# Kernel optimization log

Hardware: AMD Instinct MI355X
Metric: run time of the kernel (lower is better)

The kernel has to match this reference:

```python
import jax, jax.numpy as jnp
import numpy as np

E, N, C, A, S, H, HD, RH = 320000, 20000, 128, 4, 16, 8, 32, 64
AH = H * HD  # 256 attn-head channels; mul_alpha = AH, mul_alpha_head = HD
OUT = 128


def smooth_leaky_relu(x, a=0.2):
    # Equiformer SmoothLeakyReLU: 0.5*((1+a)*x + (1-a)*x*(2*sigmoid(x)-1))
    return 0.5 * ((1 + a) * x + (1 - a) * x * (2.0 * jax.nn.sigmoid(x) - 1.0))


def setup_inputs() -> dict:
    key = jax.random.key(0)
    ks = jax.random.split(key, 20)
    d = {
        'message': jax.random.normal(ks[0], (E, C), jnp.float32),
        'edge_attr': jax.random.normal(ks[1], (E, A), jnp.float32),
        'edge_scalars': jax.random.normal(ks[2], (E, S), jnp.float32),
        'w_rad1': jax.random.normal(ks[3], (S, RH), jnp.float32) / np.sqrt(S),
        'b_rad1': jnp.zeros((RH,), jnp.float32),
        'w_rad2': jax.random.normal(ks[4], (RH, C * A), jnp.float32) / np.sqrt(RH),
        'b_rad2': jnp.zeros((C * A,), jnp.float32),
        'w_dtp_v': jax.random.normal(ks[5], (C, A), jnp.float32) / np.sqrt(A),
        'w_lin_act': jax.random.normal(ks[6], (C, C), jnp.float32) / np.sqrt(C),
        'b_lin_act': jnp.zeros((C,), jnp.float32),
        'w_alpha': jax.random.normal(ks[7], (C, AH), jnp.float32) / np.sqrt(C),
        'b_alpha': jnp.zeros((AH,), jnp.float32),
        'w_lin_v': jax.random.normal(ks[8], (C, AH), jnp.float32) / np.sqrt(C),
        'b_lin_v': jnp.zeros((AH,), jnp.float32),
        'alpha_dot': jax.random.normal(ks[9], (H, HD), jnp.float32) / np.sqrt(HD),
        'w_proj': jax.random.normal(ks[10], (AH, OUT), jnp.float32) / np.sqrt(AH),
        'b_proj': jnp.zeros((OUT,), jnp.float32),
        'edge_dst': jax.random.randint(ks[11], (E,), 0, N, jnp.int32),
        'n_nodes_dst': N,
    }
    return d


def reference(message, edge_attr, edge_scalars,
              w_rad1, b_rad1, w_rad2, b_rad2,
              w_dtp_v, w_lin_act, b_lin_act,
              w_alpha, b_alpha, w_lin_v, b_lin_v,
              alpha_dot, w_proj, b_proj,
              edge_dst, n_nodes_dst):
    n = n_nodes_dst
    # dtp_rad: radial MLP -> per-edge depthwise TP weights [E, C, A]
    h = jax.nn.silu(edge_scalars @ w_rad1 + b_rad1)
    w = (h @ w_rad2 + b_rad2).reshape(-1, C, A)
    # sep_act.dtp (scalar irreps): out[e,c] = msg[e,c] * sum_a w[e,c,a]*attr[e,a]
    msg = message * jnp.einsum('eca,ea->ec', w, edge_attr)
    # sep_alpha -> alpha heads [E, H, HD]
    alpha = (msg @ w_alpha + b_alpha).reshape(-1, H, HD)
    # sep_act.lin + gate (scalars -> SiLU)
    value = jax.nn.silu(msg @ w_lin_act + b_lin_act)
    # sep_value: internal-weight dtp then linear, reshape to heads
    value = value * jnp.einsum('ca,ea->ec', w_dtp_v, edge_attr)
    value = (value @ w_lin_v + b_lin_v).reshape(-1, H, HD)
    # attention logits
    alpha = smooth_leaky_relu(alpha)
    alpha = jnp.einsum('ehk,hk->eh', alpha, alpha_dot)
    # scatter softmax over destination nodes
    amax = jax.ops.segment_max(alpha, edge_dst, num_segments=n)  # [N, H]
    amax = jnp.where(jnp.isfinite(amax), amax, 0.0)
    ex = jnp.exp(alpha - amax[edge_dst])
    denom = jax.ops.segment_sum(ex, edge_dst, num_segments=n)
    alpha = ex / (denom[edge_dst] + 1e-16)
    # weighted scatter-add aggregation
    attn = value * alpha[..., None]  # [E, H, HD]
    node = jax.ops.segment_sum(attn, edge_dst, num_segments=n)  # [N, H, HD]
    node = node.reshape(n, AH)  # heads2vec
    return node @ w_proj + b_proj
```

## Files before the change

### kernel.cpp

```cpp
#include <hip/hip_runtime.h>

#define C_   128
#define A_   4
#define S_   16
#define RH_  64
#define H_   8
#define AH_  256
#define OUT_ 128

typedef __attribute__((ext_vector_type(8))) short bf16x8;
typedef __attribute__((ext_vector_type(4))) float f32x4;

__device__ __forceinline__ float sigf(float x) { return 1.0f / (1.0f + __expf(-x)); }

__device__ __forceinline__ unsigned short f2bf(float x) {
    unsigned u = __float_as_uint(x);
    unsigned r = (u + 0x7fffu + ((u >> 16) & 1u)) >> 16;
    return (unsigned short)r;
}

__device__ __forceinline__ unsigned enc(float x) {
    unsigned b = __float_as_uint(x);
    return (b & 0x80000000u) ? ~b : (b | 0x80000000u);
}
__device__ __forceinline__ float dec(unsigned u) {
    unsigned b = (u & 0x80000000u) ? (u & 0x7fffffffu) : ~u;
    return __uint_as_float(b);
}

__global__ void k_pack(const float* __restrict__ W, short* __restrict__ out, int K, int N) {
    const int KS = K / 32;
    const int ct = blockIdx.x / KS, ks = blockIdx.x % KS;
    const int l = threadIdx.x, lr = l & 15, lg = l >> 4;
    bf16x8 v;
    #pragma unroll
    for (int j = 0; j < 8; j++)
        v[j] = (short)f2bf(W[(size_t)(ks * 32 + lg * 8 + j) * N + ct * 16 + lr]);
    *(bf16x8*)&out[((size_t)blockIdx.x * 64 + l) * 8] = v;
}

__global__ void k_pack_dtp(const float* __restrict__ W, short* __restrict__ out) {
    const int ct = blockIdx.x >> 3, ks = blockIdx.x & 7;
    const int l = threadIdx.x, lr = l & 15, lg = l >> 4;
    bf16x8 v;
    #pragma unroll
    for (int j = 0; j < 8; j++)
        v[j] = (short)f2bf(W[(size_t)(ks * 8 + lg * 2 + (j >> 2)) * 512 + (ct * 16 + lr) * 4 + (j & 3)]);
    *(bf16x8*)&out[((size_t)blockIdx.x * 64 + l) * 8] = v;
}

__global__ __launch_bounds__(256) void k_hist(
    const int* __restrict__ edge_dst, int* __restrict__ deg, int E)
{
    const int e = blockIdx.x * 256 + threadIdx.x;
    if (e < E) atomicAdd(&deg[edge_dst[e]], 1);
}

__global__ __launch_bounds__(1024) void k_scan(
    const int* __restrict__ deg, int* __restrict__ base, int* __restrict__ cursor, int N)
{
    __shared__ int part[1024];
    const int t = threadIdx.x;
    const int per = (N + 1023) / 1024;
    const int i0 = t * per;
    int s = 0;
    for (int i = 0; i < per; i++) { int idx = i0 + i; if (idx < N) s += deg[idx]; }
    part[t] = s;
    __syncthreads();
    for (int off = 1; off < 1024; off <<= 1) {
        int v = (t >= off) ? part[t - off] : 0;
        __syncthreads();
        part[t] += v;
        __syncthreads();
    }
    int excl = (t == 0) ? 0 : part[t - 1];
    for (int i = 0; i < per; i++) {
        int idx = i0 + i;
        if (idx < N) { base[idx] = excl; cursor[idx] = excl; excl += deg[idx]; }
    }
}

__global__ __launch_bounds__(256) void k_fill(
    const int* __restrict__ edge_dst, int* __restrict__ cursor,
    int* __restrict__ sorted, int E)
{
    const int e = blockIdx.x * 256 + threadIdx.x;
    if (e < E) {
        const int pos = atomicAdd(&cursor[edge_dst[e]], 1);
        sorted[pos] = e;
    }
}

__global__ __launch_bounds__(512, 4) void k_msgalpha(
    const float* __restrict__ message, const float* __restrict__ edge_attr,
    const float* __restrict__ edge_scalars,
    const float* __restrict__ w_rad1, const float* __restrict__ b_rad1,
    const short* __restrict__ w_rad2_lin, const float* __restrict__ b_rad2,
    const short* __restrict__ w_alpha_lin, const float* __restrict__ b_alpha,
    const float* __restrict__ alpha_dot, const int* __restrict__ edge_dst,
    short* __restrict__ msg_bf, float* __restrict__ logits, unsigned* __restrict__ amax_u)
{
    __shared__ __align__(16) char smem[50432];
    short* Ap     = (short*)smem;
    short* msg_s  = (short*)(smem + 32768);
    float* w1_s   = (float*)(smem + 32768);
    float* es_s   = (float*)(smem + 32768 + 4096);
    float* attr_s = (float*)(smem + 49152);
    int*   dst_s  = (int*)(smem + 50176);

    const int t = threadIdx.x;
    const long e0 = (long)blockIdx.x * 64;

    if (t < 256) {
        *(float4*)&w1_s[t * 4] = *(const float4*)&w_rad1[t * 4];
    } else {
        const int i = t - 256, r = i >> 2, s4 = (i & 3) * 4;
        *(float4*)&es_s[r * 17 + s4] = *(const float4*)&edge_scalars[(e0 + r) * S_ + s4];
    }
    if (t < 64) {
        *(float4*)&attr_s[t * 4] = *(const float4*)&edge_attr[(e0 + t) * A_];
        dst_s[t] = edge_dst[e0 + t];
    }
    __syncthreads();

    {
        const int r = t & 63, o0 = (t >> 6) * 8;
        float acc[8];
        #pragma unroll
        for (int i = 0; i < 8; i++) acc[i] = b_rad1[o0 + i];
        #pragma unroll
        for (int s = 0; s < S_; s++) {
            const float ev = es_s[r * 17 + s];
            #pragma unroll
            for (int i = 0; i < 8; i++) acc[i] += ev * w1_s[s * 64 + o0 + i];
        }
        float h[8];
        #pragma unroll
        for (int i = 0; i < 8; i++) { const float x = acc[i]; h[i] = x * sigf(x); }
        const float4 a4 = *(const float4*)&attr_s[r * 4];
        char* base = (char*)Ap + r * 512;
        const int sw = (r & 31) << 4;
        #pragma unroll
        for (int c = 0; c < 4; c++) {
            const float h0 = h[2 * c], h1 = h[2 * c + 1];
            bf16x8 v;
            v[0] = (short)f2bf(h0 * a4.x); v[1] = (short)f2bf(h0 * a4.y);
            v[2] = (short)f2bf(h0 * a4.z); v[3] = (short)f2bf(h0 * a4.w);
            v[4] = (short)f2bf(h1 * a4.x); v[5] = (short)f2bf(h1 * a4.y);
            v[6] = (short)f2bf(h1 * a4.z); v[7] = (short)f2bf(h1 * a4.w);
            *(bf16x8*)(base + ((o0 * 8 + c * 16) ^ sw)) = v;
        }
    }
    __syncthreads();

    const int w = t >> 6, l = t & 63, lr = l & 15, lg = l >> 4;

    {
        bf16x8 bf[8];
        #pragma unroll
        for (int ks = 0; ks < 8; ks++)
            bf[ks] = *(const bf16x8*)&w_rad2_lin[((size_t)(w * 8 + ks) * 64 + l) * 8];
        const int col = w * 16 + lr;
        const float4 b2 = *(const float4*)&b_rad2[col * 4];
        #pragma unroll 1
        for (int rt = 0; rt < 4; rt++) {
            const int arow = rt * 16 + lr;
            const char* abase = (char*)Ap + arow * 512;
            const int asw = (arow & 31) << 4;
            bf16x8 af[8];
            #pragma unroll
            for (int ks = 0; ks < 8; ks++)
                af[ks] = *(const bf16x8*)(abase + ((ks * 64 + lg * 16) ^ asw));
            f32x4 acc = {0.f, 0.f, 0.f, 0.f};
            #pragma unroll
            for (int ks = 0; ks < 8; ks++)
                acc = __builtin_amdgcn_mfma_f32_16x16x32_bf16(af[ks], bf[ks], acc, 0, 0, 0);
            #pragma unroll
            for (int r = 0; r < 4; r++) {
                const int row = rt * 16 + lg * 4 + r;
                const float4 a4 = *(const float4*)&attr_s[row * 4];
                const float badj = a4.x * b2.x + a4.y * b2.y + a4.z * b2.z + a4.w * b2.w;
                const float m = message[(e0 + row) * C_ + col];
                *(short*)((char*)msg_s + row * 256 + ((col * 2) ^ ((row & 15) << 4))) =
                    (short)f2bf(m * (acc[r] + badj));
            }
        }
    }
    __syncthreads();

    {
        #pragma unroll
        for (int i = 0; i < 2; i++) {
            const int q = t + i * 512;
            const int row = q >> 4, ch = q & 15;
            const uint4 v = *(const uint4*)((char*)msg_s + row * 256 + ((ch * 16) ^ ((row & 15) << 4)));
            *(uint4*)((char*)msg_bf + ((e0 + row) * 256 + ch * 16)) = v;
        }
    }

    {
        bf16x8 waf[2][4];
        float4 ba4[2], ad4[2];
        #pragma unroll
        for (int q = 0; q < 2; q++) {
            const int rt = w * 2 + q;
            #pragma unroll
            for (int ks = 0; ks < 4; ks++)
                waf[q][ks] = *(const bf16x8*)&w_alpha_lin[((size_t)(rt * 4 + ks) * 64 + l) * 8];
            ba4[q] = *(const float4*)&b_alpha[rt * 16 + lg * 4];
            ad4[q] = *(const float4*)&alpha_dot[rt * 16 + lg * 4];
        }
        #pragma unroll 1
        for (int ct = 0; ct < 4; ct++) {
            const int erow = ct * 16 + lr;
            const char* mbase = (char*)msg_s + erow * 256;
            const int msw = (erow & 15) << 4;
            bf16x8 mb[4];
            #pragma unroll
            for (int ks = 0; ks < 4; ks++)
                mb[ks] = *(const bf16x8*)(mbase + ((ks * 64 + lg * 16) ^ msw));
            float s = 0.f;
            #pragma unroll
            for (int q = 0; q < 2; q++) {
                f32x4 acc = {0.f, 0.f, 0.f, 0.f};
                #pragma unroll
                for (int ks = 0; ks < 4; ks++)
                    acc = __builtin_amdgcn_mfma_f32_16x16x32_bf16(waf[q][ks], mb[ks], acc, 0, 0, 0);
                #pragma unroll
                for (int r = 0; r < 4; r++) {
                    const float x = acc[r] + ((const float*)&ba4[q])[r];
                    const float y = x * (0.2f + 0.8f * sigf(x));
                    s += y * ((const float*)&ad4[q])[r];
                }
            }
            s += __shfl_xor(s, 16);
            s += __shfl_xor(s, 32);
            if (lg == 0) {
                const long e = e0 + ct * 16 + lr;
                logits[e * H_ + w] = s;
                atomicMax(&amax_u[dst_s[ct * 16 + lr] * H_ + w], enc(s));
            }
        }
    }
}

__global__ __launch_bounds__(256) void k_denom(
    const float* __restrict__ logits, const int* __restrict__ edge_dst,
    const unsigned* __restrict__ amax_u, float* __restrict__ denom, int EH)
{
    const int t = blockIdx.x * 256 + threadIdx.x;
    if (t >= EH) return;
    const int e = t >> 3, h = t & 7;
    const int n = edge_dst[e];
    const float am = dec(amax_u[n * H_ + h]);
    atomicAdd(&denom[n * H_ + h], __expf(logits[t] - am));
}

__global__ __launch_bounds__(256) void k_value(
    const short* __restrict__ msg_bf, const float* __restrict__ edge_attr,
    const short* __restrict__ w_lin_act_lin, const float* __restrict__ b_lin_act,
    const float* __restrict__ w_dtp_v,
    const short* __restrict__ w_lin_v_lin, const float* __restrict__ b_lin_v,
    const float* __restrict__ logits, const int* __restrict__ edge_dst,
    const unsigned* __restrict__ amax_u, const float* __restrict__ denom,
    const int* __restrict__ sorted, float* __restrict__ node)
{
    __shared__ __align__(16) short a_s[32 * 128];
    __shared__ __align__(16) short v_s[32 * 128];
    __shared__ float val2[32 * 260];
    __shared__ float attr_s[32][4];
    __shared__ float wgt_s[32][H_];
    __shared__ int   dst_s[32];
    __shared__ int   eid_s[32];
    const int t = threadIdx.x;
    const int b0 = blockIdx.x * 32;

    if (t < 32) {
        const int e = sorted[b0 + t];
        eid_s[t] = e;
        dst_s[t] = edge_dst[e];
        *(float4*)&attr_s[t][0] = *(const float4*)&edge_attr[(long)e * A_];
    }
    __syncthreads();
    #pragma unroll
    for (int i = 0; i < 2; i++) {
        const int row = (t >> 4) + i * 16, ch = t & 15;
        const uint4 v = *(const uint4*)((const char*)msg_bf + ((long)eid_s[row] * 256 + ch * 16));
        *(uint4*)((char*)a_s + row * 256 + ((ch * 16) ^ ((row & 7) << 4))) = v;
    }
    {
        const int el = t >> 3, h = t & 7;
        const long e = eid_s[el];
        const int n = dst_s[el];
        const float am = dec(amax_u[n * H_ + h]);
        const float d  = denom[n * H_ + h];
        wgt_s[el][h] = __expf(logits[e * H_ + h] - am) / (d + 1e-16f);
    }
    __syncthreads();

    const int w = t >> 6, l = t & 63, lr = l & 15, lg = l >> 4;
    bf16x8 af[2][4];
    #pragma unroll
    for (int rt = 0; rt < 2; rt++)
        #pragma unroll
        for (int ks = 0; ks < 4; ks++) {
            const int row = rt * 16 + lr;
            af[rt][ks] = *(bf16x8*)((char*)a_s + row * 256 + ((ks * 64 + lg * 16) ^ ((row & 7) << 4)));
        }
    #pragma unroll
    for (int q = 0; q < 2; q++) {
        const int ct = w * 2 + q;
        bf16x8 bf[4];
        #pragma unroll
        for (int ks = 0; ks < 4; ks++)
            bf[ks] = *(const bf16x8*)&w_lin_act_lin[((size_t)(ct * 4 + ks) * 64 + l) * 8];
        const int col = ct * 16 + lr;
        const float bb = b_lin_act[col];
        const float4 wv = *(const float4*)&w_dtp_v[col * 4];
        #pragma unroll
        for (int rt = 0; rt < 2; rt++) {
            f32x4 acc = {0.f, 0.f, 0.f, 0.f};
            #pragma unroll
            for (int ks = 0; ks < 4; ks++)
                acc = __builtin_amdgcn_mfma_f32_16x16x32_bf16(af[rt][ks], bf[ks], acc, 0, 0, 0);
            #pragma unroll
            for (int r = 0; r < 4; r++) {
                const int row = rt * 16 + lg * 4 + r;
                float x = acc[r] + bb;
                x = x * sigf(x);
                const float4 a4 = *(const float4*)&attr_s[row][0];
                const float dv = wv.x * a4.x + wv.y * a4.y + wv.z * a4.z + wv.w * a4.w;
                *(short*)((char*)v_s + row * 256 + ((col * 2) ^ ((row & 7) << 4))) =
                    (short)f2bf(x * dv);
            }
        }
    }
    __syncthreads();

    bf16x8 vf[2][4];
    #pragma unroll
    for (int rt = 0; rt < 2; rt++)
        #pragma unroll
        for (int ks = 0; ks < 4; ks++) {
            const int row = rt * 16 + lr;
            vf[rt][ks] = *(bf16x8*)((char*)v_s + row * 256 + ((ks * 64 + lg * 16) ^ ((row & 7) << 4)));
        }
    #pragma unroll
    for (int q = 0; q < 4; q++) {
        const int ct = w * 4 + q;
        bf16x8 bf[4];
        #pragma unroll
        for (int ks = 0; ks < 4; ks++)
            bf[ks] = *(const bf16x8*)&w_lin_v_lin[((size_t)(ct * 4 + ks) * 64 + l) * 8];
        const int col = ct * 16 + lr;
        const float bb = b_lin_v[col];
        #pragma unroll
        for (int rt = 0; rt < 2; rt++) {
            f32x4 acc = {0.f, 0.f, 0.f, 0.f};
            #pragma unroll
            for (int ks = 0; ks < 4; ks++)
                acc = __builtin_amdgcn_mfma_f32_16x16x32_bf16(vf[rt][ks], bf[ks], acc, 0, 0, 0);
            #pragma unroll
            for (int r = 0; r < 4; r++) {
                const int row = rt * 16 + lg * 4 + r;
                val2[row * 260 + col] = (acc[r] + bb) * wgt_s[row][col >> 5];
            }
        }
    }
    __syncthreads();
    {
        const int c = t;
        float run = 0.f;
        int s = 0;
        #pragma unroll 1
        for (int e = 0; e < 32; e++) {
            run += val2[e * 260 + c];
            const bool end = (e == 31) || (dst_s[e + 1] != dst_s[e]);
            if (end) {
                float* np = node + (long)dst_s[e] * AH_ + c;
                if (s == 0 || e == 31) atomicAdd(np, run);
                else *np = run;
                run = 0.f; s = e + 1;
            }
        }
    }
}

__global__ __launch_bounds__(256) void k_proj(
    const float* __restrict__ node, const float* __restrict__ w_proj,
    const float* __restrict__ b_proj, float* __restrict__ out)
{
    __shared__ float node_s[32][AH_];
    const int t = threadIdx.x;
    const long n0 = (long)blockIdx.x * 32;
    #pragma unroll
    for (int i = 0; i < 8; i++) {
        const int idx = t + i * 256;
        const int nl = idx >> 6, c4 = (idx & 63) * 4;
        *(float4*)&node_s[nl][c4] = *(const float4*)&node[(n0 + nl) * AH_ + c4];
    }
    __syncthreads();
    const int j0 = (t & 31) * 4;
    const int g  = t >> 5;
    float4 acc4[4];
    const float4 b = *(const float4*)&b_proj[j0];
    #pragma unroll
    for (int i = 0; i < 4; i++) acc4[i] = b;
    const float* wp = w_proj + j0;
    for (int c4 = 0; c4 < 64; c4++) {
        const float4 w0 = *(const float4*)&wp[(c4 * 4 + 0) * OUT_];
        const float4 w1 = *(const float4*)&wp[(c4 * 4 + 1) * OUT_];
        const float4 w2 = *(const float4*)&wp[(c4 * 4 + 2) * OUT_];
        const float4 w3 = *(const float4*)&wp[(c4 * 4 + 3) * OUT_];
        #pragma unroll
        for (int i = 0; i < 4; i++) {
            const float4 nv = *(const float4*)&node_s[g * 4 + i][c4 * 4];
            acc4[i].x += nv.x * w0.x + nv.y * w1.x + nv.z * w2.x + nv.w * w3.x;
            acc4[i].y += nv.x * w0.y + nv.y * w1.y + nv.z * w2.y + nv.w * w3.y;
            acc4[i].z += nv.x * w0.z + nv.y * w1.z + nv.z * w2.z + nv.w * w3.z;
            acc4[i].w += nv.x * w0.w + nv.y * w1.w + nv.z * w2.w + nv.w * w3.w;
        }
    }
    #pragma unroll
    for (int i = 0; i < 4; i++) {
        const long n = n0 + g * 4 + i;
        *(float4*)&out[n * OUT_ + j0] = acc4[i];
    }
}

extern "C" void kernel_launch(void* const* d_in, const int* in_sizes, int n_in,
                              void* d_out, int out_size, void* d_ws, size_t ws_size,
                              hipStream_t stream)
{
    const float* message      = (const float*)d_in[0];
    const float* edge_attr    = (const float*)d_in[1];
    const float* edge_scalars = (const float*)d_in[2];
    const float* w_rad1       = (const float*)d_in[3];
    const float* b_rad1       = (const float*)d_in[4];
    const float* w_rad2       = (const float*)d_in[5];
    const float* b_rad2       = (const float*)d_in[6];
    const float* w_dtp_v      = (const float*)d_in[7];
    const float* w_lin_act    = (const float*)d_in[8];
    const float* b_lin_act    = (const float*)d_in[9];
    const float* w_alpha      = (const float*)d_in[10];
    const float* b_alpha      = (const float*)d_in[11];
    const float* w_lin_v      = (const float*)d_in[12];
    const float* b_lin_v      = (const float*)d_in[13];
    const float* alpha_dot    = (const float*)d_in[14];
    const float* w_proj       = (const float*)d_in[15];
    const float* b_proj       = (const float*)d_in[16];
    const int*   edge_dst     = (const int*)d_in[17];

    const int E = in_sizes[0] / C_;
    const int N = out_size / OUT_;

    char* ws = (char*)d_ws;
    float*    node     = (float*)ws;
    unsigned* amax_u   = (unsigned*)(node + (size_t)N * AH_);
    float*    denom    = (float*)(amax_u + (size_t)N * H_);
    int*      deg      = (int*)(denom + (size_t)N * H_);
    int*      base     = deg + N;
    int*      cursor   = base + N;
    int*      sorted   = cursor + N;
    short*    w_rad2_l = (short*)(sorted + E);
    short*    w_alph_l = w_rad2_l + 64 * 512;
    short*    w_lact_l = w_alph_l + 128 * 256;
    short*    w_linv_l = w_lact_l + 128 * 128;
    short*    msg_bf   = w_linv_l + 128 * 256;
    float*    logits   = (float*)(msg_bf + (size_t)E * C_);

    hipMemsetAsync(d_ws, 0, (size_t)N * (AH_ + 2 * H_ + 1) * 4, stream);

    const int nbE256 = (E + 255) / 256;
    k_pack_dtp<<<64, 64, 0, stream>>>(w_rad2, w_rad2_l);
    k_pack<<<(256/16)*(128/32), 64, 0, stream>>>(w_alpha,   w_alph_l, 128, 256);
    k_pack<<<(128/16)*(128/32), 64, 0, stream>>>(w_lin_act, w_lact_l, 128, 128);
    k_pack<<<(256/16)*(128/32), 64, 0, stream>>>(w_lin_v,   w_linv_l, 128, 256);
    k_hist<<<nbE256, 256, 0, stream>>>(edge_dst, deg, E);
    k_scan<<<1, 1024, 0, stream>>>(deg, base, cursor, N);
    k_fill<<<nbE256, 256, 0, stream>>>(edge_dst, cursor, sorted, E);
    k_msgalpha<<<E / 64, 512, 0, stream>>>(message, edge_attr, edge_scalars,
                                           w_rad1, b_rad1, w_rad2_l, b_rad2,
                                           w_alph_l, b_alpha, alpha_dot, edge_dst,
                                           msg_bf, logits, amax_u);
    k_denom<<<(E * H_ + 255) / 256, 256, 0, stream>>>(logits, edge_dst, amax_u, denom, E * H_);
    k_value<<<E / 32, 256, 0, stream>>>(msg_bf, edge_attr, w_lact_l, b_lin_act, w_dtp_v,
                                        w_linv_l, b_lin_v, logits, edge_dst, amax_u, denom,
                                        sorted, node);
    k_proj<<<N / 32, 256, 0, stream>>>(node, w_proj, b_proj, (float*)d_out);
}
```

Before: 423.9 us.

## Double k_value edge tile to 64 with 512 threads and alias LDS buffers

```diff
diff --git a/kernel.cpp b/kernel.cpp
--- a/kernel.cpp
+++ b/kernel.cpp
@@ -1,4 +1,5 @@
 #include <hip/hip_runtime.h>
+#include <hip/hip_bf16.h>
 
 #define C_   128
 #define A_   4
@@ -17,6 +18,12 @@
     unsigned u = __float_as_uint(x);
     unsigned r = (u + 0x7fffu + ((u >> 16) & 1u)) >> 16;
     return (unsigned short)r;
+}
+
+__device__ __forceinline__ unsigned pkbf(float a, float b) {
+    union { __hip_bfloat162 h; unsigned u; } c;
+    c.h = __float22bfloat162_rn(float2{a, b});
+    return c.u;
 }
 
 __device__ __forceinline__ unsigned enc(float x) {
@@ -143,12 +150,12 @@
         #pragma unroll
         for (int c = 0; c < 4; c++) {
             const float h0 = h[2 * c], h1 = h[2 * c + 1];
-            bf16x8 v;
-            v[0] = (short)f2bf(h0 * a4.x); v[1] = (short)f2bf(h0 * a4.y);
-            v[2] = (short)f2bf(h0 * a4.z); v[3] = (short)f2bf(h0 * a4.w);
-            v[4] = (short)f2bf(h1 * a4.x); v[5] = (short)f2bf(h1 * a4.y);
-            v[6] = (short)f2bf(h1 * a4.z); v[7] = (short)f2bf(h1 * a4.w);
-            *(bf16x8*)(base + ((o0 * 8 + c * 16) ^ sw)) = v;
+            uint4 v;
+            v.x = pkbf(h0 * a4.x, h0 * a4.y);
+            v.y = pkbf(h0 * a4.z, h0 * a4.w);
+            v.z = pkbf(h1 * a4.x, h1 * a4.y);
+            v.w = pkbf(h1 * a4.z, h1 * a4.w);
+            *(uint4*)(base + ((o0 * 8 + c * 16) ^ sw)) = v;
         }
     }
     __syncthreads();
@@ -256,7 +263,7 @@
     atomicAdd(&denom[n * H_ + h], __expf(logits[t] - am));
 }
 
-__global__ __launch_bounds__(256) void k_value(
+__global__ __launch_bounds__(512, 2) void k_value(
     const short* __restrict__ msg_bf, const float* __restrict__ edge_attr,
     const short* __restrict__ w_lin_act_lin, const float* __restrict__ b_lin_act,
     const float* __restrict__ w_dtp_v,
@@ -265,17 +272,19 @@
     const unsigned* __restrict__ amax_u, const float* __restrict__ denom,
     const int* __restrict__ sorted, float* __restrict__ node)
 {
-    __shared__ __align__(16) short a_s[32 * 128];
-    __shared__ __align__(16) short v_s[32 * 128];
-    __shared__ float val2[32 * 260];
-    __shared__ float attr_s[32][4];
-    __shared__ float wgt_s[32][H_];
-    __shared__ int   dst_s[32];
-    __shared__ int   eid_s[32];
+    __shared__ __align__(16) char pool[66560];
+    __shared__ float attr_s[64][4];
+    __shared__ float wgt_s[64][H_];
+    __shared__ int   dst_s[64];
+    __shared__ int   eid_s[64];
+    short* a_s  = (short*)pool;
+    short* v_s  = (short*)(pool + 16384);
+    float* val2 = (float*)pool;
+
     const int t = threadIdx.x;
-    const int b0 = blockIdx.x * 32;
-
-    if (t < 32) {
+    const int b0 = blockIdx.x * 64;
+
+    if (t < 64) {
         const int e = sorted[b0 + t];
         eid_s[t] = e;
         dst_s[t] = edge_dst[e];
@@ -284,9 +293,10 @@
     __syncthreads();
     #pragma unroll
     for (int i = 0; i < 2; i++) {
-        const int row = (t >> 4) + i * 16, ch = t & 15;
+        const int q = t + i * 512;
+        const int row = q >> 4, ch = q & 15;
         const uint4 v = *(const uint4*)((const char*)msg_bf + ((long)eid_s[row] * 256 + ch * 16));
-        *(uint4*)((char*)a_s + row * 256 + ((ch * 16) ^ ((row & 7) << 4))) = v;
+        *(uint4*)((char*)a_s + row * 256 + ((ch * 16) ^ ((row & 15) << 4))) = v;
     }
     {
         const int el = t >> 3, h = t & 7;
@@ -299,26 +309,24 @@
     __syncthreads();
 
     const int w = t >> 6, l = t & 63, lr = l & 15, lg = l >> 4;
-    bf16x8 af[2][4];
-    #pragma unroll
-    for (int rt = 0; rt < 2; rt++)
-        #pragma unroll
-        for (int ks = 0; ks < 4; ks++) {
-            const int row = rt * 16 + lr;
-            af[rt][ks] = *(bf16x8*)((char*)a_s + row * 256 + ((ks * 64 + lg * 16) ^ ((row & 7) << 4)));
-        }
-    #pragma unroll
-    for (int q = 0; q < 2; q++) {
-        const int ct = w * 2 + q;
+    {
+        bf16x8 af[4][4];
+        #pragma unroll
+        for (int rt = 0; rt < 4; rt++)
+            #pragma unroll
+            for (int ks = 0; ks < 4; ks++) {
+                const int row = rt * 16 + lr;
+                af[rt][ks] = *(bf16x8*)((char*)a_s + row * 256 + ((ks * 64 + lg * 16) ^ ((row & 15) << 4)));
+            }
         bf16x8 bf[4];
         #pragma unroll
         for (int ks = 0; ks < 4; ks++)
-            bf[ks] = *(const bf16x8*)&w_lin_act_lin[((size_t)(ct * 4 + ks) * 64 + l) * 8];
-        const int col = ct * 16 + lr;
+            bf[ks] = *(const bf16x8*)&w_lin_act_lin[((size_t)(w * 4 + ks) * 64 + l) * 8];
+        const int col = w * 16 + lr;
         const float bb = b_lin_act[col];
         const float4 wv = *(const float4*)&w_dtp_v[col * 4];
         #pragma unroll
-        for (int rt = 0; rt < 2; rt++) {
+        for (int rt = 0; rt < 4; rt++) {
             f32x4 acc = {0.f, 0.f, 0.f, 0.f};
             #pragma unroll
             for (int ks = 0; ks < 4; ks++)
@@ -330,24 +338,26 @@
                 x = x * sigf(x);
                 const float4 a4 = *(const float4*)&attr_s[row][0];
                 const float dv = wv.x * a4.x + wv.y * a4.y + wv.z * a4.z + wv.w * a4.w;
-                *(short*)((char*)v_s + row * 256 + ((col * 2) ^ ((row & 7) << 4))) =
+                *(short*)((char*)v_s + row * 256 + ((col * 2) ^ ((row & 15) << 4))) =
                     (short)f2bf(x * dv);
             }
         }
     }
     __syncthreads();
 
-    bf16x8 vf[2][4];
-    #pragma unroll
-    for (int rt = 0; rt < 2; rt++)
+    bf16x8 vf[4][4];
+    #pragma unroll
+    for (int rt = 0; rt < 4; rt++)
         #pragma unroll
         for (int ks = 0; ks < 4; ks++) {
             const int row = rt * 16 + lr;
-            vf[rt][ks] = *(bf16x8*)((char*)v_s + row * 256 + ((ks * 64 + lg * 16) ^ ((row & 7) << 4)));
-        }
-    #pragma unroll
-    for (int q = 0; q < 4; q++) {
-        const int ct = w * 4 + q;
+            vf[rt][ks] = *(bf16x8*)((char*)v_s + row * 256 + ((ks * 64 + lg * 16) ^ ((row & 15) << 4)));
+        }
+    __syncthreads();
+
+    #pragma unroll
+    for (int q = 0; q < 2; q++) {
+        const int ct = w * 2 + q;
         bf16x8 bf[4];
         #pragma unroll
         for (int ks = 0; ks < 4; ks++)
@@ -355,7 +365,7 @@
         const int col = ct * 16 + lr;
         const float bb = b_lin_v[col];
         #pragma unroll
-        for (int rt = 0; rt < 2; rt++) {
+        for (int rt = 0; rt < 4; rt++) {
             f32x4 acc = {0.f, 0.f, 0.f, 0.f};
             #pragma unroll
             for (int ks = 0; ks < 4; ks++)
@@ -369,16 +379,16 @@
     }
     __syncthreads();
     {
-        const int c = t;
+        const int c = t & 255, eS = (t >> 8) * 32, eE = eS + 32;
         float run = 0.f;
-        int s = 0;
+        int s = eS;
         #pragma unroll 1
-        for (int e = 0; e < 32; e++) {
+        for (int e = eS; e < eE; e++) {
             run += val2[e * 260 + c];
-            const bool end = (e == 31) || (dst_s[e + 1] != dst_s[e]);
+            const bool end = (e == eE - 1) || (dst_s[e + 1] != dst_s[e]);
             if (end) {
                 float* np = node + (long)dst_s[e] * AH_ + c;
-                if (s == 0 || e == 31) atomicAdd(np, run);
+                if (s == eS || e == eE - 1) atomicAdd(np, run);
                 else *np = run;
                 run = 0.f; s = e + 1;
             }
@@ -484,7 +494,7 @@
                                            w_alph_l, b_alpha, alpha_dot, edge_dst,
                                            msg_bf, logits, amax_u);
     k_denom<<<(E * H_ + 255) / 256, 256, 0, stream>>>(logits, edge_dst, amax_u, denom, E * H_);
-    k_value<<<E / 32, 256, 0, stream>>>(msg_bf, edge_attr, w_lact_l, b_lin_act, w_dtp_v,
+    k_value<<<E / 64, 512, 0, stream>>>(msg_bf, edge_attr, w_lact_l, b_lin_act, w_dtp_v,
                                         w_linv_l, b_lin_v, logits, edge_dst, amax_u, denom,
                                         sorted, node);
     k_proj<<<N / 32, 256, 0, stream>>>(node, w_proj, b_proj, (float*)d_out);
```

Measured after the change: 420.1 us. About the same (-0.9%).
